# Kernel optimization log

Measured on AMD Instinct MI355X. Metric: run time of the kernel, lower is better.

## Reference

```python
import jax, jax.numpy as jnp
import numpy as np


def setup_inputs() -> dict:
    key = jax.random.key(0)
    k1, k2, k3 = jax.random.split(key, 3)
    B, Cin, H, W = 64, 16, 256, 256
    Cout, K = 64, 3
    x = jax.random.normal(k1, (B, Cin, H, W), dtype=jnp.float32)
    # PyTorch Conv2d init scale ~ 1/sqrt(fan_in)
    fan_in = Cin * K * K
    conv_weight = jax.random.normal(k2, (Cout, Cin, K, K), dtype=jnp.float32) / np.sqrt(fan_in)
    conv_bias = jax.random.normal(k3, (Cout,), dtype=jnp.float32) / np.sqrt(fan_in)
    return {"x": x, "conv_weight": conv_weight, "conv_bias": conv_bias}


def reference(x, conv_weight, conv_bias):
    # Conv2d: stride=1, padding=0 (VALID), dilation=1, groups=1
    y = jax.lax.conv_general_dilated(
        x, conv_weight,
        window_strides=(1, 1),
        padding="VALID",
        dimension_numbers=("NCHW", "OIHW", "NCHW"),
    ) + conv_bias[None, :, None, None]          # [B, Cout, 254, 254]
    m = jnp.min(y, axis=1, keepdims=True)        # [B, 1, 254, 254] min over channels
    return jnp.tanh(jnp.tanh(m))                 # double tanh
```

## Files before the change

kernel.cpp:

```cpp
#include <hip/hip_runtime.h>
#include <math.h>

#define CIN    16
#define COUT   64
#define H      256
#define W      256
#define OH     254
#define OW     254
#define NTAP   9
#define RING   6
#define STRIP  32

typedef _Float16 f16x8  __attribute__((ext_vector_type(8)));
typedef float    f32x16 __attribute__((ext_vector_type(16)));

#define XSLOT(w, g) ((((w) << 1) | (g)) ^ (((w) >> 2) & 7))

__global__ void wpack_kernel(const float* __restrict__ w, _Float16* __restrict__ wpk) {
    int idx = blockIdx.x * 256 + threadIdx.x;
    if (idx >= NTAP * 2 * 64 * 8) return;
    int e = idx & 7, l = (idx >> 3) & 63, m = (idx >> 9) & 1, t = idx >> 10;
    int co  = (l & 31) + 32 * m;
    int cin = 8 * (l >> 5) + e;
    wpk[idx] = (_Float16)w[((co * CIN + cin) * 3 + t / 3) * 3 + (t % 3)];
}

__device__ __forceinline__ float tanh_fast(float v) {
    float e = __expf(2.0f * v);
    return 1.0f - 2.0f * __builtin_amdgcn_rcpf(e + 1.0f);
}

__global__ __launch_bounds__(256, 2) void conv_mfma_kernel(
        const float* __restrict__ x, const f16x8* __restrict__ wpk,
        const float* __restrict__ bias, float* __restrict__ out) {
    __shared__ f16x8 xs[RING * 512];

    const int tid = threadIdx.x;
    const int b   = blockIdx.x >> 3;
    const int s   = blockIdx.x & 7;
    const int oh0 = s * STRIP;

    const float* xb = x + (size_t)b * CIN * H * W;
    const int lane = tid & 63;

    f16x8 wreg[NTAP][2];
#pragma unroll
    for (int t = 0; t < NTAP; ++t)
#pragma unroll
        for (int m = 0; m < 2; ++m)
            wreg[t][m] = wpk[(t * 2 + m) * 64 + lane];

    const int wave = tid >> 6;
    const int ph   = wave * 64;
    const int l31  = lane & 31;
    const int g2   = lane >> 5;

    f32x16 cbias[2];
#pragma unroll
    for (int m = 0; m < 2; ++m)
#pragma unroll
        for (int r = 0; r < 16; ++r)
            cbias[m][r] = bias[(r & 3) + 8 * (r >> 2) + 4 * g2 + 32 * m];

    int off[3][2];
#pragma unroll
    for (int kw = 0; kw < 3; ++kw)
#pragma unroll
        for (int n = 0; n < 2; ++n) {
            int w = ph + 32 * n + l31 + kw;
            if (w > 255) w = 255;
            off[kw][n] = XSLOT(w, g2);
        }

#define STAGE_LOAD(rowAbs, v)                                                   \
    {                                                                           \
        int row_ = (rowAbs) > 255 ? 255 : (rowAbs);                             \
        const float* p_ = xb + (size_t)row_ * W + tid;                          \
        _Pragma("unroll")                                                       \
        for (int c = 0; c < CIN; ++c) v[c] = p_[(size_t)c * (H * W)];           \
    }
#define STAGE_WRITE(slot, v)                                                    \
    {                                                                           \
        f16x8 q0, q1;                                                           \
        _Pragma("unroll")                                                       \
        for (int c = 0; c < 8; ++c) { q0[c] = (_Float16)v[c];                   \
                                      q1[c] = (_Float16)v[c + 8]; }             \
        xs[(slot) * 512 + XSLOT(tid, 0)] = q0;                                  \
        xs[(slot) * 512 + XSLOT(tid, 1)] = q1;                                  \
    }

#pragma unroll
    for (int i = 0; i < 4; ++i) {
        float v[CIN];
        STAGE_LOAD(oh0 + i, v)
        STAGE_WRITE(i, v)
    }
    __syncthreads();

    int rs0 = 0, rs1 = 1, rs2 = 2, wsl = 4;

    for (int r = 0; r < STRIP; ++r) {
        float v[CIN];
        STAGE_LOAD(oh0 + r + 4, v)

        const f16x8* x0 = xs + rs0 * 512;
        const f16x8* x1 = xs + rs1 * 512;
        const f16x8* x2 = xs + rs2 * 512;

        f32x16 acc[2][2];
#pragma unroll
        for (int t = 0; t < NTAP; ++t) {
            const int kh = t / 3, kw = t % 3;
            const f16x8* xr = (kh == 0) ? x0 : (kh == 1) ? x1 : x2;
#pragma unroll
            for (int n = 0; n < 2; ++n) {
                f16x8 bf = xr[off[kw][n]];
                if (t == 0) {
                    acc[0][n] = __builtin_amdgcn_mfma_f32_32x32x16_f16(wreg[0][0], bf, cbias[0], 0, 0, 0);
                    acc[1][n] = __builtin_amdgcn_mfma_f32_32x32x16_f16(wreg[0][1], bf, cbias[1], 0, 0, 0);
                } else {
                    acc[0][n] = __builtin_amdgcn_mfma_f32_32x32x16_f16(wreg[t][0], bf, acc[0][n], 0, 0, 0);
                    acc[1][n] = __builtin_amdgcn_mfma_f32_32x32x16_f16(wreg[t][1], bf, acc[1][n], 0, 0, 0);
                }
            }
        }

        const int oh = oh0 + r;
#pragma unroll
        for (int n = 0; n < 2; ++n) {
            float mn = fminf(acc[0][n][0], acc[1][n][0]);
#pragma unroll
            for (int q = 1; q < 16; ++q)
                mn = fminf(mn, fminf(acc[0][n][q], acc[1][n][q]));
            mn = fminf(mn, __shfl_xor(mn, 32));
            float t2 = tanh_fast(tanh_fast(mn));
            int px = ph + 32 * n + l31;
            if (g2 == 0 && px < OW && oh < OH)
                out[((size_t)b * OH + oh) * OW + px] = t2;
        }

        STAGE_WRITE(wsl, v)

        if (r & 1) __syncthreads();

        rs0 = (rs0 == RING - 1) ? 0 : rs0 + 1;
        rs1 = (rs1 == RING - 1) ? 0 : rs1 + 1;
        rs2 = (rs2 == RING - 1) ? 0 : rs2 + 1;
        wsl = (wsl == RING - 1) ? 0 : wsl + 1;
    }
}

extern "C" void kernel_launch(void* const* d_in, const int* in_sizes, int n_in,
                              void* d_out, int out_size, void* d_ws, size_t ws_size,
                              hipStream_t stream) {
    const float* x    = (const float*)d_in[0];
    const float* w    = (const float*)d_in[1];
    const float* bias = (const float*)d_in[2];
    float* out = (float*)d_out;
    _Float16* wpk = (_Float16*)d_ws;

    wpack_kernel<<<36, 256, 0, stream>>>(w, wpk);
    conv_mfma_kernel<<<64 * 8, 256, 0, stream>>>(x, (const f16x8*)wpk, bias, out);
}
```

Before: 94.37 us.

## Tile conv as 128-pixel column halves with two output rows per iteration

Each block now covers a 128-column half and 64 output rows instead of a full-width 32-row strip, and computes two output rows per iteration so each staged input row fragment is reused across both rows' MFMAs. Staging uses float2 loads split across channel groups, with a halo lane loading the extra columns, a new XOR swizzle and an 8-slot ring. Block IDs are remapped to interleave batches. The aim is fewer LDS reads per MFMA and fewer barriers per output row. In exchange, halo columns are loaded twice and a halo-duty lane adds divergence.

After: 97.14 us. 2.9% more time.

```diff
diff --git a/kernel.cpp b/kernel.cpp
--- a/kernel.cpp
+++ b/kernel.cpp
@@ -8,13 +8,14 @@
 #define OH     254
 #define OW     254
 #define NTAP   9
-#define RING   6
-#define STRIP  32
+#define RING   8
+#define SROW   264
+#define NIT    32
 
 typedef _Float16 f16x8  __attribute__((ext_vector_type(8)));
 typedef float    f32x16 __attribute__((ext_vector_type(16)));
 
-#define XSLOT(w, g) ((((w) << 1) | (g)) ^ (((w) >> 2) & 7))
+#define XP(px) ((px) ^ (((px) >> 3) & 7))
 
 __global__ void wpack_kernel(const float* __restrict__ w, _Float16* __restrict__ wpk) {
     int idx = blockIdx.x * 256 + threadIdx.x;
@@ -29,19 +30,26 @@
     float e = __expf(2.0f * v);
     return 1.0f - 2.0f * __builtin_amdgcn_rcpf(e + 1.0f);
 }
+__device__ __forceinline__ float min3f(float a, float b, float c) {
+    return fminf(fminf(a, b), c);
+}
 
 __global__ __launch_bounds__(256, 2) void conv_mfma_kernel(
         const float* __restrict__ x, const f16x8* __restrict__ wpk,
         const float* __restrict__ bias, float* __restrict__ out) {
-    __shared__ f16x8 xs[RING * 512];
+    __shared__ f16x8 xs[RING * SROW];
 
-    const int tid = threadIdx.x;
-    const int b   = blockIdx.x >> 3;
-    const int s   = blockIdx.x & 7;
-    const int oh0 = s * STRIP;
+    const int tid  = threadIdx.x;
+    const int lane = tid & 63;
+
+    int bid = blockIdx.x;
+    int nb  = (bid & 7) * 64 + (bid >> 3);
+    int b   = nb >> 3;
+    int rem = nb & 7;
+    const int P0 = (rem & 1) * 128;
+    const int r0 = (rem >> 1) * 64;
 
     const float* xb = x + (size_t)b * CIN * H * W;
-    const int lane = tid & 63;
 
     f16x8 wreg[NTAP][2];
 #pragma unroll
@@ -51,9 +59,61 @@
             wreg[t][m] = wpk[(t * 2 + m) * 64 + lane];
 
     const int wave = tid >> 6;
-    const int ph   = wave * 64;
     const int l31  = lane & 31;
     const int g2   = lane >> 5;
+
+    const int sr = tid >> 7;
+    const int sg = (tid >> 6) & 1;
+    const int sp = tid & 63;
+    const bool hduty = (sp == 63);
+
+    float2 vm[8];
+    float2 vh[8];
+
+#define SLOAD(dRel)                                                             \
+    {                                                                           \
+        int row_ = r0 + (dRel); if (row_ > 255) row_ = 255;                     \
+        const float* p_ = xb + (size_t)row_ * W;                                \
+        _Pragma("unroll")                                                       \
+        for (int c = 0; c < 8; ++c)                                             \
+            vm[c] = *(const float2*)(p_ + (size_t)(8 * sg + c) * (H * W) + P0 + 2 * sp); \
+        if (hduty) {                                                            \
+            int hp_ = P0 + 128; if (hp_ > 254) hp_ = 254;                       \
+            _Pragma("unroll")                                                   \
+            for (int c = 0; c < 8; ++c)                                         \
+                vh[c] = *(const float2*)(p_ + (size_t)(8 * sg + c) * (H * W) + hp_); \
+        }                                                                       \
+    }
+
+#define SWRITE(slot)                                                            \
+    {                                                                           \
+        f16x8 q0, q1;                                                           \
+        _Pragma("unroll")                                                       \
+        for (int c = 0; c < 8; ++c) { q0[c] = (_Float16)vm[c].x;                \
+                                      q1[c] = (_Float16)vm[c].y; }              \
+        f16x8* base_ = xs + (slot) * SROW + sg * 132;                           \
+        base_[XP(2 * sp)]     = q0;                                             \
+        base_[XP(2 * sp + 1)] = q1;                                             \
+        if (hduty) {                                                            \
+            f16x8 h0, h1;                                                       \
+            _Pragma("unroll")                                                   \
+            for (int c = 0; c < 8; ++c) { h0[c] = (_Float16)vh[c].x;            \
+                                          h1[c] = (_Float16)vh[c].y; }          \
+            base_[XP(128)] = h0;                                                \
+            base_[XP(129)] = h1;                                                \
+        }                                                                       \
+    }
+
+#pragma unroll
+    for (int j = 0; j < 3; ++j) {
+        SLOAD(2 * j + sr)
+        SWRITE(2 * j + sr)
+    }
+
+    int roff[3];
+#pragma unroll
+    for (int kw = 0; kw < 3; ++kw)
+        roff[kw] = g2 * 132 + XP(32 * wave + l31 + kw);
 
     f32x16 cbias[2];
 #pragma unroll
@@ -62,91 +122,52 @@
         for (int r = 0; r < 16; ++r)
             cbias[m][r] = bias[(r & 3) + 8 * (r >> 2) + 4 * g2 + 32 * m];
 
-    int off[3][2];
-#pragma unroll
-    for (int kw = 0; kw < 3; ++kw)
-#pragma unroll
-        for (int n = 0; n < 2; ++n) {
-            int w = ph + 32 * n + l31 + kw;
-            if (w > 255) w = 255;
-            off[kw][n] = XSLOT(w, g2);
-        }
-
-#define STAGE_LOAD(rowAbs, v)                                                   \
-    {                                                                           \
-        int row_ = (rowAbs) > 255 ? 255 : (rowAbs);                             \
-        const float* p_ = xb + (size_t)row_ * W + tid;                          \
-        _Pragma("unroll")                                                       \
-        for (int c = 0; c < CIN; ++c) v[c] = p_[(size_t)c * (H * W)];           \
-    }
-#define STAGE_WRITE(slot, v)                                                    \
-    {                                                                           \
-        f16x8 q0, q1;                                                           \
-        _Pragma("unroll")                                                       \
-        for (int c = 0; c < 8; ++c) { q0[c] = (_Float16)v[c];                   \
-                                      q1[c] = (_Float16)v[c + 8]; }             \
-        xs[(slot) * 512 + XSLOT(tid, 0)] = q0;                                  \
-        xs[(slot) * 512 + XSLOT(tid, 1)] = q1;                                  \
-    }
-
-#pragma unroll
-    for (int i = 0; i < 4; ++i) {
-        float v[CIN];
-        STAGE_LOAD(oh0 + i, v)
-        STAGE_WRITE(i, v)
-    }
     __syncthreads();
 
-    int rs0 = 0, rs1 = 1, rs2 = 2, wsl = 4;
-
-    for (int r = 0; r < STRIP; ++r) {
-        float v[CIN];
-        STAGE_LOAD(oh0 + r + 4, v)
-
-        const f16x8* x0 = xs + rs0 * 512;
-        const f16x8* x1 = xs + rs1 * 512;
-        const f16x8* x2 = xs + rs2 * 512;
+#pragma unroll 1
+    for (int i = 0; i < NIT; ++i) {
+        const bool pf = (i < 30);
+        if (pf) SLOAD(2 * i + 6 + sr)
 
         f32x16 acc[2][2];
 #pragma unroll
-        for (int t = 0; t < NTAP; ++t) {
-            const int kh = t / 3, kw = t % 3;
-            const f16x8* xr = (kh == 0) ? x0 : (kh == 1) ? x1 : x2;
+        for (int dd = 0; dd < 4; ++dd) {
+            const f16x8* xr = xs + ((2 * i + dd) & 7) * SROW;
+            f16x8 f0 = xr[roff[0]];
+            f16x8 f1 = xr[roff[1]];
+            f16x8 f2 = xr[roff[2]];
 #pragma unroll
-            for (int n = 0; n < 2; ++n) {
-                f16x8 bf = xr[off[kw][n]];
-                if (t == 0) {
-                    acc[0][n] = __builtin_amdgcn_mfma_f32_32x32x16_f16(wreg[0][0], bf, cbias[0], 0, 0, 0);
-                    acc[1][n] = __builtin_amdgcn_mfma_f32_32x32x16_f16(wreg[0][1], bf, cbias[1], 0, 0, 0);
-                } else {
-                    acc[0][n] = __builtin_amdgcn_mfma_f32_32x32x16_f16(wreg[t][0], bf, acc[0][n], 0, 0, 0);
-                    acc[1][n] = __builtin_amdgcn_mfma_f32_32x32x16_f16(wreg[t][1], bf, acc[1][n], 0, 0, 0);
+            for (int ro = 0; ro < 2; ++ro) {
+                const int kh = dd - ro;
+                if (kh < 0 || kh > 2) continue;
+#pragma unroll
+                for (int m = 0; m < 2; ++m) {
+                    if (kh == 0)
+                        acc[ro][m] = __builtin_amdgcn_mfma_f32_32x32x16_f16(wreg[0][m], f0, cbias[m], 0, 0, 0);
+                    else
+                        acc[ro][m] = __builtin_amdgcn_mfma_f32_32x32x16_f16(wreg[kh * 3][m], f0, acc[ro][m], 0, 0, 0);
+                    acc[ro][m] = __builtin_amdgcn_mfma_f32_32x32x16_f16(wreg[kh * 3 + 1][m], f1, acc[ro][m], 0, 0, 0);
+                    acc[ro][m] = __builtin_amdgcn_mfma_f32_32x32x16_f16(wreg[kh * 3 + 2][m], f2, acc[ro][m], 0, 0, 0);
                 }
             }
         }
 
-        const int oh = oh0 + r;
+        __syncthreads();
+        if (pf) SWRITE((2 * i + 6 + sr) & 7)
+
 #pragma unroll
-        for (int n = 0; n < 2; ++n) {
-            float mn = fminf(acc[0][n][0], acc[1][n][0]);
+        for (int ro = 0; ro < 2; ++ro) {
+            const int oh = r0 + 2 * i + ro;
+            float mn = fminf(acc[ro][0][0], acc[ro][1][0]);
 #pragma unroll
             for (int q = 1; q < 16; ++q)
-                mn = fminf(mn, fminf(acc[0][n][q], acc[1][n][q]));
+                mn = min3f(acc[ro][0][q], acc[ro][1][q], mn);
             mn = fminf(mn, __shfl_xor(mn, 32));
             float t2 = tanh_fast(tanh_fast(mn));
-            int px = ph + 32 * n + l31;
+            const int px = P0 + 32 * wave + l31;
             if (g2 == 0 && px < OW && oh < OH)
                 out[((size_t)b * OH + oh) * OW + px] = t2;
         }
-
-        STAGE_WRITE(wsl, v)
-
-        if (r & 1) __syncthreads();
-
-        rs0 = (rs0 == RING - 1) ? 0 : rs0 + 1;
-        rs1 = (rs1 == RING - 1) ? 0 : rs1 + 1;
-        rs2 = (rs2 == RING - 1) ? 0 : rs2 + 1;
-        wsl = (wsl == RING - 1) ? 0 : wsl + 1;
     }
 }
 
@@ -160,5 +181,5 @@
     _Float16* wpk = (_Float16*)d_ws;
 
     wpack_kernel<<<36, 256, 0, stream>>>(w, wpk);
-    conv_mfma_kernel<<<64 * 8, 256, 0, stream>>>(x, (const f16x8*)wpk, bias, out);
+    conv_mfma_kernel<<<512, 256, 0, stream>>>(x, (const f16x8*)wpk, bias, out);
 }
```
